# Optimization experiments

Hardware: AMD Instinct MI355X
Metric: run time of the kernel (lower is better)

The kernel has to match this reference:

```python
import jax, jax.numpy as jnp
import numpy as np

B, DIM, T, H = 8, 1024, 2048, 16
HD = DIM // H  # per-head channel dim = 64


def _toeplitz(v):
    # v: (H, T) -> (H, T, T) with M[h, i, j] = v[h, j - i] if j >= i else 0
    m = v.shape[-1]
    i = jnp.arange(m)[:, None]
    j = jnp.arange(m)[None, :]
    idx = jnp.where(j >= i, j - i, 0)
    return jnp.where(j >= i, v[..., idx], jnp.zeros((), v.dtype))


def setup_inputs() -> dict:
    key = jax.random.key(0)
    ks = jax.random.split(key, 5)
    s = 1.0 / np.sqrt(DIM)
    return {
        "x": jax.random.normal(ks[0], (B, DIM, T), jnp.float32),
        "w_in": jax.random.normal(ks[1], (DIM, DIM), jnp.float32) * s,
        "b_in": jnp.zeros((DIM,), jnp.float32),
        "w_out": jax.random.normal(ks[2], (DIM, DIM), jnp.float32) * s,
        "b_out": jnp.zeros((DIM,), jnp.float32),
        "toep_w": jax.random.normal(ks[3], (H, T), jnp.float32) * 0.02,
        "toep_b": jnp.zeros((H, T), jnp.float32),
    }


def reference(x, w_in, b_in, w_out, b_out, toep_w, toep_b):
    # x: (B, DIM, T) -> (B, T, DIM)
    xt = jnp.transpose(x, (0, 2, 1))
    h1 = xt @ w_in.T + b_in  # (B, T, DIM)
    # (B, T, H*HD) -> (B, H, HD, T)
    p = jnp.transpose(h1.reshape(B, T, H, HD), (0, 2, 3, 1))
    M = _toeplitz(toep_w)  # (H, T, T)
    # bmm with per-head causal Toeplitz matrix + per-head bias over time
    conv = jnp.einsum("bhdt,htu->bhdu", p, M) + toep_b[None, :, None, :]
    # (B, H, HD, T) -> (B, T, H*HD)
    merged = jnp.transpose(conv, (0, 3, 1, 2)).reshape(B, T, DIM)
    out = merged @ w_out.T + b_out  # (B, T, DIM)
    return jnp.transpose(out, (0, 2, 1))  # (B, DIM, T)
```

## Files before the change

### kernel.cpp

```cpp
#include <hip/hip_runtime.h>
#include <hip/hip_bf16.h>
#include <stdint.h>

#define B_   8
#define DIM  1024
#define T_   2048
#define H_   16
#define HD   64

typedef __attribute__((ext_vector_type(8))) short bf16x8;
typedef __attribute__((ext_vector_type(4))) float f32x4;
typedef __attribute__((ext_vector_type(4))) unsigned short u16x4;

__device__ __forceinline__ unsigned short f2bf(float f) {
    union { float f; unsigned u; } v{f};
    unsigned r = v.u + 0x7fffu + ((v.u >> 16) & 1u);
    return (unsigned short)(r >> 16);
}

__device__ __forceinline__ void gl_lds16(const unsigned short* g, unsigned short* l) {
    __builtin_amdgcn_global_load_lds(
        (const __attribute__((address_space(1))) void*)(const void*)g,
        (__attribute__((address_space(3))) void*)(void*)l,
        16, 0, 0);
}

__device__ __forceinline__ bf16x8 ld_frag(const unsigned short* smem, int row, int cg) {
    return *reinterpret_cast<const bf16x8*>(smem + row * 64 + (((cg) ^ (row & 7)) << 3));
}

__global__ void xpose_cast(const float* __restrict__ x, unsigned short* __restrict__ xt) {
    __shared__ float tile[64][65];
    const int b = blockIdx.z;
    const int d0 = blockIdx.y * 64, t0 = blockIdx.x * 64;
    const int tid = threadIdx.x;
    const int c = tid & 63;
    const int r0 = tid >> 6;

    const float* xp = x + ((size_t)b * DIM + d0) * T_ + t0;
#pragma unroll
    for (int i = 0; i < 16; ++i) {
        int r = r0 + i * 4;
        tile[r][c] = xp[(size_t)r * T_ + c];
    }
    __syncthreads();
    unsigned short* op = xt + ((size_t)b * T_ + t0) * DIM + d0;
    const int ci = (tid & 15) * 4;
    const int rr = tid >> 4;
#pragma unroll
    for (int i = 0; i < 4; ++i) {
        int r = rr + i * 16;
        u16x4 v;
#pragma unroll
        for (int j = 0; j < 4; ++j) v[j] = f2bf(tile[ci + j][r]);
        *reinterpret_cast<u16x4*>(op + (size_t)r * DIM + ci) = v;
    }
}

__global__ void cast_weights(const float* __restrict__ w_in, const float* __restrict__ w_out,
                             unsigned short* __restrict__ w_in_b, unsigned short* __restrict__ w_out_b) {
    int i = blockIdx.x * 256 + threadIdx.x;
    if (i < DIM * DIM) {
        w_in_b[i]  = f2bf(w_in[i]);
        w_out_b[i] = f2bf(w_out[i]);
    }
}

__global__ void gen_mfrag(const float* __restrict__ tw, unsigned short* __restrict__ Mf) {
    const int h = blockIdx.y, dg = blockIdx.x;
    const int D = (dg - 1) * 64;
    const float* twh = tw + h * T_;
    unsigned short* out = Mf + (((size_t)h * 32 + dg) << 13);
    for (int v = threadIdx.x; v < 1024; v += 256) {
        int cg = v >> 7, row = v & 127;
        bf16x8 w;
#pragma unroll
        for (int j = 0; j < 8; ++j) {
            int lag = D + row - (cg * 8 + j);
            w[j] = (lag >= 0) ? (short)f2bf(twh[lag]) : (short)0;
        }
        *reinterpret_cast<bf16x8*>(out + (size_t)v * 8) = w;
    }
}

template <bool OUT_BF16>
__global__ void gemm_k(const unsigned short* __restrict__ Aw,
                       const unsigned short* __restrict__ Bm,
                       const float* __restrict__ bias,
                       void* __restrict__ Out) {
    __shared__ __align__(16) unsigned short As[128 * 64];
    __shared__ __align__(16) unsigned short Bs[128 * 64];

    const int flat = blockIdx.x;
    const int wid  = (flat & 7) * 128 + (flat >> 3);
    const int nx   = wid & 15;
    const int my   = (wid >> 4) & 7;
    const int b    = wid >> 7;

    const int tid = threadIdx.x, lane = tid & 63, wv = tid >> 6;
    const int m0 = my * 128;
    const int n0 = nx * 128;
    const unsigned short* Bb = Bm + (size_t)b * T_ * DIM;

    const int wr = wv >> 1, wc = wv & 1;
    const int lrow = lane & 15, lg = lane >> 4;

    f32x4 acc[4][4] = {};

    for (int k0 = 0; k0 < DIM; k0 += 64) {
        __syncthreads();
#pragma unroll
        for (int it = 0; it < 4; ++it) {
            int ch = wv * 4 + it;
            int r  = ch * 8 + (lane >> 3);
            int g  = (lane & 7) ^ (lane >> 3);
            gl_lds16(Aw + (size_t)(m0 + r) * DIM + k0 + g * 8, As + ch * 512);
            gl_lds16(Bb + (size_t)(n0 + r) * DIM + k0 + g * 8, Bs + ch * 512);
        }
        __syncthreads();

#pragma unroll
        for (int kk = 0; kk < 2; ++kk) {
            bf16x8 af[4], bfr[4];
#pragma unroll
            for (int mt = 0; mt < 4; ++mt) af[mt]  = ld_frag(As, wr * 64 + mt * 16 + lrow, kk * 4 + lg);
#pragma unroll
            for (int nt = 0; nt < 4; ++nt) bfr[nt] = ld_frag(Bs, wc * 64 + nt * 16 + lrow, kk * 4 + lg);
#pragma unroll
            for (int mt = 0; mt < 4; ++mt)
#pragma unroll
                for (int nt = 0; nt < 4; ++nt)
                    acc[mt][nt] = __builtin_amdgcn_mfma_f32_16x16x32_bf16(af[mt], bfr[nt], acc[mt][nt], 0, 0, 0);
        }
    }

    const size_t ob = (size_t)b * DIM * T_;
#pragma unroll
    for (int mt = 0; mt < 4; ++mt) {
        int d = m0 + wr * 64 + mt * 16 + lg * 4;
#pragma unroll
        for (int nt = 0; nt < 4; ++nt) {
            int t = n0 + wc * 64 + nt * 16 + lrow;
#pragma unroll
            for (int r = 0; r < 4; ++r) {
                float v = acc[mt][nt][r] + bias[d + r];
                if constexpr (OUT_BF16)
                    ((unsigned short*)Out)[ob + (size_t)(d + r) * T_ + t] = f2bf(v);
                else
                    ((float*)Out)[ob + (size_t)(d + r) * T_ + t] = v;
            }
        }
    }
}

__global__ void conv6_k(const unsigned short* __restrict__ H1,
                        const unsigned short* __restrict__ Mf,
                        const float* __restrict__ tb,
                        unsigned short* __restrict__ Cb) {
    __shared__ __align__(16) unsigned short Ps[2][128 * 64];

    const int flat = blockIdx.x;
    const int wid  = (flat & 7) * 64 + (flat >> 3);
    const int bx   = wid & 7;
    const int bp   = (wid >> 3) & 3;
    const int h    = wid >> 5;
    const int b0   = bp * 2;

    const int tid = threadIdx.x, lane = tid & 63, wv = tid >> 6;
    const unsigned short* Hb0 = H1 + ((size_t)b0 * DIM + h * HD) * T_;
    const unsigned short* Hb1 = H1 + ((size_t)(b0 + 1) * DIM + h * HD) * T_;
    const unsigned short* Ah  = Mf + ((size_t)h * 32) * 8192;

    const int lrow = lane & 15, lg = lane >> 4;
    const int rsub = lane >> 3;
    const int g = (lane & 7) ^ rsub;

    const int aoff = (lg * 128 + wv * 32 + lrow) * 8;

    auto PSTAGE = [&](int kt, int p) {
        const int t0 = kt * 64;
#pragma unroll
        for (int it = 0; it < 4; ++it) {
            int ch = wv * 4 + it;
            int r  = ch * 8 + rsub;
            const unsigned short* src = (r < 64)
                ? (Hb0 + (size_t)r * T_ + t0 + g * 8)
                : (Hb1 + (size_t)(r - 64) * T_ + t0 + g * 8);
            gl_lds16(src, &Ps[p][0] + ch * 512);
        }
    };

#pragma unroll
    for (int ph = 0; ph < 2; ++ph) {
        const int ut = ph ? bx : (T_ / 128 - 1 - bx);
        const int u0 = ut * 128;
        const int nk = 2 * ut + 2;
        f32x4 acc[2][8] = {};

        PSTAGE(0, 0);
        __syncthreads();

        for (int kt = 0; kt < nk; ++kt) {
            const int cur = kt & 1;
            if (kt + 1 < nk) PSTAGE(kt + 1, cur ^ 1);

            const int dg = 2 * ut - kt + 1;
            const unsigned short* At = Ah + (size_t)dg * 8192;
            bf16x8 af0[2], af1[2];
#pragma unroll
            for (int mt = 0; mt < 2; ++mt) {
                af0[mt] = *reinterpret_cast<const bf16x8*>(At + aoff + mt * 128);
                af1[mt] = *reinterpret_cast<const bf16x8*>(At + 4096 + aoff + mt * 128);
            }
            const unsigned short* Pb = &Ps[cur][0];
            bf16x8 bfr[8];
#pragma unroll
            for (int nt = 0; nt < 8; ++nt) bfr[nt] = ld_frag(Pb, nt * 16 + lrow, lg);
#pragma unroll
            for (int mt = 0; mt < 2; ++mt)
#pragma unroll
                for (int nt = 0; nt < 8; ++nt)
                    acc[mt][nt] = __builtin_amdgcn_mfma_f32_16x16x32_bf16(af0[mt], bfr[nt], acc[mt][nt], 0, 0, 0);
#pragma unroll
            for (int nt = 0; nt < 8; ++nt) bfr[nt] = ld_frag(Pb, nt * 16 + lrow, 4 + lg);
#pragma unroll
            for (int mt = 0; mt < 2; ++mt)
#pragma unroll
                for (int nt = 0; nt < 8; ++nt)
                    acc[mt][nt] = __builtin_amdgcn_mfma_f32_16x16x32_bf16(af1[mt], bfr[nt], acc[mt][nt], 0, 0, 0);

            __syncthreads();
        }

#pragma unroll
        for (int mt = 0; mt < 2; ++mt) {
            int u = u0 + wv * 32 + mt * 16 + lg * 4;
            const float* tbp = tb + h * T_ + u;
            float t0v = tbp[0], t1v = tbp[1], t2v = tbp[2], t3v = tbp[3];
#pragma unroll
            for (int nt = 0; nt < 8; ++nt) {
                int col = nt * 16 + lrow;
                int bb  = b0 + (col >> 6);
                int d   = col & 63;
                size_t p = (size_t)bb * T_ * DIM + (size_t)u * DIM + (size_t)h * HD + d;
                Cb[p]           = f2bf(acc[mt][nt][0] + t0v);
                Cb[p + DIM]     = f2bf(acc[mt][nt][1] + t1v);
                Cb[p + 2 * DIM] = f2bf(acc[mt][nt][2] + t2v);
                Cb[p + 3 * DIM] = f2bf(acc[mt][nt][3] + t3v);
            }
        }
    }
}

extern "C" void kernel_launch(void* const* d_in, const int* in_sizes, int n_in,
                              void* d_out, int out_size, void* d_ws, size_t ws_size,
                              hipStream_t stream) {
    (void)in_sizes; (void)n_in; (void)out_size; (void)ws_size;
    const float* x      = (const float*)d_in[0];
    const float* w_in   = (const float*)d_in[1];
    const float* b_in   = (const float*)d_in[2];
    const float* w_out  = (const float*)d_in[3];
    const float* b_out  = (const float*)d_in[4];
    const float* toep_w = (const float*)d_in[5];
    const float* toep_b = (const float*)d_in[6];

    char* ws = (char*)d_ws;
    unsigned short* XT    = (unsigned short*)(ws);
    unsigned short* H1    = (unsigned short*)(ws + 33554432);
    unsigned short* Cbuf  = (unsigned short*)(ws + 67108864);
    unsigned short* winb  = (unsigned short*)(ws + 100663296);
    unsigned short* woutb = (unsigned short*)(ws + 102760448);
    unsigned short* Mfrag = (unsigned short*)(ws + 104857600);

    xpose_cast<<<dim3(T_ / 64, DIM / 64, B_), dim3(256), 0, stream>>>(x, XT);
    cast_weights<<<dim3((DIM * DIM) / 256), dim3(256), 0, stream>>>(w_in, w_out, winb, woutb);
    gen_mfrag<<<dim3(32, H_), dim3(256), 0, stream>>>(toep_w, Mfrag);
    gemm_k<true><<<dim3(1024), dim3(256), 0, stream>>>(winb, XT, b_in, (void*)H1);
    conv6_k<<<dim3(512), dim3(256), 0, stream>>>(H1, Mfrag, toep_b, Cbuf);
    gemm_k<false><<<dim3(1024), dim3(256), 0, stream>>>(woutb, Cbuf, b_out, d_out);
}
```

Before: 160.1 us.

## Retile Toeplitz conv kernel to one batch per block with 2-wave blocks

The conv kernel now gives each block a single batch instead of a pair, using 128 threads (2 waves) and twice as many blocks. Each wave computes a 64x64 tile (4x4 MFMA fragments) rather than 32x128, so fewer Toeplitz A fragments are reused across batches and the P tile in LDS is halved. The aim is more blocks for occupancy and load balance across CUs, at the cost of reading the Toeplitz fragments twice as often from global memory.

```diff
diff --git a/kernel.cpp b/kernel.cpp
--- a/kernel.cpp
+++ b/kernel.cpp
@@ -153,29 +153,28 @@
     }
 }
 
-__global__ void conv6_k(const unsigned short* __restrict__ H1,
-                        const unsigned short* __restrict__ Mf,
-                        const float* __restrict__ tb,
-                        unsigned short* __restrict__ Cb) {
-    __shared__ __align__(16) unsigned short Ps[2][128 * 64];
+__global__ __launch_bounds__(128)
+void conv7_k(const unsigned short* __restrict__ H1,
+             const unsigned short* __restrict__ Mf,
+             const float* __restrict__ tb,
+             unsigned short* __restrict__ Cb) {
+    __shared__ __align__(16) unsigned short Ps[2][64 * 64];
 
     const int flat = blockIdx.x;
-    const int wid  = (flat & 7) * 64 + (flat >> 3);
+    const int wid  = (flat & 7) * 128 + (flat >> 3);
     const int bx   = wid & 7;
-    const int bp   = (wid >> 3) & 3;
-    const int h    = wid >> 5;
-    const int b0   = bp * 2;
+    const int b    = (wid >> 3) & 7;
+    const int h    = wid >> 6;
 
     const int tid = threadIdx.x, lane = tid & 63, wv = tid >> 6;
-    const unsigned short* Hb0 = H1 + ((size_t)b0 * DIM + h * HD) * T_;
-    const unsigned short* Hb1 = H1 + ((size_t)(b0 + 1) * DIM + h * HD) * T_;
-    const unsigned short* Ah  = Mf + ((size_t)h * 32) * 8192;
+    const unsigned short* Hb = H1 + ((size_t)b * DIM + h * HD) * T_;
+    const unsigned short* Ah = Mf + ((size_t)h * 32) * 8192;
 
     const int lrow = lane & 15, lg = lane >> 4;
     const int rsub = lane >> 3;
     const int g = (lane & 7) ^ rsub;
 
-    const int aoff = (lg * 128 + wv * 32 + lrow) * 8;
+    const int aoff = (lg * 128 + wv * 64 + lrow) * 8;
 
     auto PSTAGE = [&](int kt, int p) {
         const int t0 = kt * 64;
@@ -183,10 +182,7 @@
         for (int it = 0; it < 4; ++it) {
             int ch = wv * 4 + it;
             int r  = ch * 8 + rsub;
-            const unsigned short* src = (r < 64)
-                ? (Hb0 + (size_t)r * T_ + t0 + g * 8)
-                : (Hb1 + (size_t)(r - 64) * T_ + t0 + g * 8);
-            gl_lds16(src, &Ps[p][0] + ch * 512);
+            gl_lds16(Hb + (size_t)r * T_ + t0 + g * 8, &Ps[p][0] + ch * 512);
         }
     };
 
@@ -195,7 +191,7 @@
         const int ut = ph ? bx : (T_ / 128 - 1 - bx);
         const int u0 = ut * 128;
         const int nk = 2 * ut + 2;
-        f32x4 acc[2][8] = {};
+        f32x4 acc[4][4] = {};
 
         PSTAGE(0, 0);
         __syncthreads();
@@ -206,43 +202,48 @@
 
             const int dg = 2 * ut - kt + 1;
             const unsigned short* At = Ah + (size_t)dg * 8192;
-            bf16x8 af0[2], af1[2];
-#pragma unroll
-            for (int mt = 0; mt < 2; ++mt) {
-                af0[mt] = *reinterpret_cast<const bf16x8*>(At + aoff + mt * 128);
-                af1[mt] = *reinterpret_cast<const bf16x8*>(At + 4096 + aoff + mt * 128);
-            }
             const unsigned short* Pb = &Ps[cur][0];
-            bf16x8 bfr[8];
-#pragma unroll
-            for (int nt = 0; nt < 8; ++nt) bfr[nt] = ld_frag(Pb, nt * 16 + lrow, lg);
-#pragma unroll
-            for (int mt = 0; mt < 2; ++mt)
-#pragma unroll
-                for (int nt = 0; nt < 8; ++nt)
-                    acc[mt][nt] = __builtin_amdgcn_mfma_f32_16x16x32_bf16(af0[mt], bfr[nt], acc[mt][nt], 0, 0, 0);
-#pragma unroll
-            for (int nt = 0; nt < 8; ++nt) bfr[nt] = ld_frag(Pb, nt * 16 + lrow, 4 + lg);
-#pragma unroll
-            for (int mt = 0; mt < 2; ++mt)
-#pragma unroll
-                for (int nt = 0; nt < 8; ++nt)
-                    acc[mt][nt] = __builtin_amdgcn_mfma_f32_16x16x32_bf16(af1[mt], bfr[nt], acc[mt][nt], 0, 0, 0);
+
+            {
+                bf16x8 af[4], bfr[4];
+#pragma unroll
+                for (int mt = 0; mt < 4; ++mt)
+                    af[mt] = *reinterpret_cast<const bf16x8*>(At + aoff + mt * 128);
+#pragma unroll
+                for (int nt = 0; nt < 4; ++nt) bfr[nt] = ld_frag(Pb, nt * 16 + lrow, lg);
+#pragma unroll
+                for (int mt = 0; mt < 4; ++mt)
+#pragma unroll
+                    for (int nt = 0; nt < 4; ++nt)
+                        acc[mt][nt] = __builtin_amdgcn_mfma_f32_16x16x32_bf16(af[mt], bfr[nt], acc[mt][nt], 0, 0, 0);
+            }
+            {
+                bf16x8 af[4], bfr[4];
+#pragma unroll
+                for (int mt = 0; mt < 4; ++mt)
+                    af[mt] = *reinterpret_cast<const bf16x8*>(At + 4096 + aoff + mt * 128);
+#pragma unroll
+                for (int nt = 0; nt < 4; ++nt) bfr[nt] = ld_frag(Pb, nt * 16 + lrow, 4 + lg);
+#pragma unroll
+                for (int mt = 0; mt < 4; ++mt)
+#pragma unroll
+                    for (int nt = 0; nt < 4; ++nt)
+                        acc[mt][nt] = __builtin_amdgcn_mfma_f32_16x16x32_bf16(af[mt], bfr[nt], acc[mt][nt], 0, 0, 0);
+            }
 
             __syncthreads();
         }
 
-#pragma unroll
-        for (int mt = 0; mt < 2; ++mt) {
-            int u = u0 + wv * 32 + mt * 16 + lg * 4;
+        const size_t base = (size_t)b * T_ * DIM + (size_t)h * HD;
+#pragma unroll
+        for (int mt = 0; mt < 4; ++mt) {
+            int u = u0 + wv * 64 + mt * 16 + lg * 4;
             const float* tbp = tb + h * T_ + u;
             float t0v = tbp[0], t1v = tbp[1], t2v = tbp[2], t3v = tbp[3];
 #pragma unroll
-            for (int nt = 0; nt < 8; ++nt) {
-                int col = nt * 16 + lrow;
-                int bb  = b0 + (col >> 6);
-                int d   = col & 63;
-                size_t p = (size_t)bb * T_ * DIM + (size_t)u * DIM + (size_t)h * HD + d;
+            for (int nt = 0; nt < 4; ++nt) {
+                int d = nt * 16 + lrow;
+                size_t p = base + (size_t)u * DIM + d;
                 Cb[p]           = f2bf(acc[mt][nt][0] + t0v);
                 Cb[p + DIM]     = f2bf(acc[mt][nt][1] + t1v);
                 Cb[p + 2 * DIM] = f2bf(acc[mt][nt][2] + t2v);
@@ -276,6 +277,6 @@
     cast_weights<<<dim3((DIM * DIM) / 256), dim3(256), 0, stream>>>(w_in, w_out, winb, woutb);
     gen_mfrag<<<dim3(32, H_), dim3(256), 0, stream>>>(toep_w, Mfrag);
     gemm_k<true><<<dim3(1024), dim3(256), 0, stream>>>(winb, XT, b_in, (void*)H1);
-    conv6_k<<<dim3(512), dim3(256), 0, stream>>>(H1, Mfrag, toep_b, Cbuf);
+    conv7_k<<<dim3(1024), dim3(128), 0, stream>>>(H1, Mfrag, toep_b, Cbuf);
     gemm_k<false><<<dim3(1024), dim3(256), 0, stream>>>(woutb, Cbuf, b_out, d_out);
 }
```

New measurement: 154.4 us. 1.04x faster.
